# Optimization experiments

Measured on AMD Instinct MI355X. Metric: run time of the kernel, lower is better.

The kernel has to match this reference:

```python
import jax, jax.numpy as jnp
import numpy as np

B, C = 1048576, 40
ALPHA = 0.5          # additive offset so distance factor is never 0
NORMALISE = 1.0      # opt['hier_normalise']


def setup_inputs() -> dict:
    key = jax.random.key(0)
    k1, k2, k3 = jax.random.split(key, 3)
    logits = jax.random.normal(k1, (B, C), dtype=jnp.float32)
    labels = jax.random.randint(k2, (B,), 0, C, dtype=jnp.int32)
    dis_matrix = jax.random.uniform(k3, (C, C), dtype=jnp.float32)
    return {"logits": logits, "labels": labels, "dis_matrix": dis_matrix}


def reference(logits, labels, dis_matrix):
    # per-sample cross entropy (reduction='none')
    logp = jax.nn.log_softmax(logits, axis=-1)                      # [B, C]
    ce = -jnp.take_along_axis(logp, labels[:, None].astype(jnp.int32), axis=-1)[:, 0]  # [B]
    # argmax predictions (done on host in the original; pure gather here)
    pred = jnp.argmax(logits, axis=-1)                              # [B]
    # distance_factor = DIS_MATRIX[gold, pred] + alpha   (non-LCA path)
    distance_factor = dis_matrix[labels, pred] + ALPHA              # [B]
    total_loss = jnp.mean(ce * distance_factor) / NORMALISE
    return total_loss, distance_factor
```

## Files before the change

kernel.cpp:

```cpp
#include <hip/hip_runtime.h>
#include <hip/hip_bf16.h>


#define HDL_B 1048576
#define HDL_C 40
#define HDL_ALPHA 0.5f
#define HDL_BLOCK 256
#define HDL_GRID (HDL_B / HDL_BLOCK)

__global__ __launch_bounds__(HDL_BLOCK)
void hdl_main(const float* __restrict__ logits,
              const int* __restrict__ labels,
              const float* __restrict__ dis,
              float* __restrict__ out,
              double* __restrict__ wsum_global) {
    __shared__ float dls[HDL_C * HDL_C];
    __shared__ float wpart[HDL_BLOCK / 64];

    for (int i = threadIdx.x; i < HDL_C * HDL_C; i += HDL_BLOCK)
        dls[i] = dis[i];
    __syncthreads();

    const int row = blockIdx.x * HDL_BLOCK + threadIdx.x;

    const float4* rp = reinterpret_cast<const float4*>(logits + (size_t)row * HDL_C);
    float x[HDL_C];
#pragma unroll
    for (int k = 0; k < HDL_C / 4; ++k) {
        float4 t = rp[k];
        x[4 * k + 0] = t.x;
        x[4 * k + 1] = t.y;
        x[4 * k + 2] = t.z;
        x[4 * k + 3] = t.w;
    }

    float m = x[0];
    int pred = 0;
#pragma unroll
    for (int j = 1; j < HDL_C; ++j) {
        bool g = x[j] > m;
        m = g ? x[j] : m;
        pred = g ? j : pred;
    }

    const float L2E = 1.4426950408889634f;
    const float mL = m * L2E;
    float s = 0.0f;
#pragma unroll
    for (int j = 0; j < HDL_C; ++j)
        s += __builtin_amdgcn_exp2f(__builtin_fmaf(x[j], L2E, -mL));

    const int lab = labels[row];
    const float xl = logits[(size_t)row * HDL_C + lab];

    const float ce = (m - xl) + 0.69314718055994531f * __builtin_amdgcn_logf(s);

    const float df = dls[lab * HDL_C + pred] + HDL_ALPHA;
    out[1 + row] = df;

    float val = ce * df;

#pragma unroll
    for (int o = 32; o > 0; o >>= 1)
        val += __shfl_down(val, o, 64);
    const int lane = threadIdx.x & 63;
    const int wid = threadIdx.x >> 6;
    if (lane == 0) wpart[wid] = val;
    __syncthreads();
    if (threadIdx.x == 0) {
        float bs = wpart[0] + wpart[1] + wpart[2] + wpart[3];
        atomicAdd(wsum_global, (double)bs);
    }
}

__global__ void hdl_finalize(const double* __restrict__ wsum_global,
                             float* __restrict__ out) {
    out[0] = (float)(wsum_global[0] * (1.0 / (double)HDL_B));
}

extern "C" void kernel_launch(void* const* d_in, const int* in_sizes, int n_in,
                              void* d_out, int out_size, void* d_ws, size_t ws_size,
                              hipStream_t stream) {
    const float* logits = (const float*)d_in[0];
    const int*   labels = (const int*)d_in[1];
    const float* dis    = (const float*)d_in[2];
    float* out = (float*)d_out;
    double* wsum = (double*)d_ws;

    hipMemsetAsync(wsum, 0, sizeof(double), stream);

    hdl_main<<<HDL_GRID, HDL_BLOCK, 0, stream>>>(logits, labels, dis, out, wsum);
    hdl_finalize<<<1, 1, 0, stream>>>(wsum, out);
}
```

Baseline: 249.7 us.

## Stage logits through padded shared-memory tiles and replace atomic with two-pass reduction

Logits are now loaded by the whole block as consecutive float4s, so the global reads are fully coalesced, and staged through a padded shared tile in two halves before each thread pulls its own row. The label logit comes from the tile instead of a second scattered global read. The shared copy of the distance matrix is removed and it is read directly from global memory. The per-block double atomic and the memset are replaced by per-block partial sums that a 256-thread finalize kernel reduces. This adds two extra block barriers and more shared-memory traffic per block.

```diff
diff --git a/kernel.cpp b/kernel.cpp
--- a/kernel.cpp
+++ b/kernel.cpp
@@ -6,39 +6,63 @@
 #define HDL_C 40
 #define HDL_ALPHA 0.5f
 #define HDL_BLOCK 256
-#define HDL_GRID (HDL_B / HDL_BLOCK)
+#define HDL_ROWS 256
+#define HDL_GRID (HDL_B / HDL_ROWS)
+#define HDL_HALF 128
+#define HDL_PAD 41
 
 __global__ __launch_bounds__(HDL_BLOCK)
 void hdl_main(const float* __restrict__ logits,
               const int* __restrict__ labels,
               const float* __restrict__ dis,
               float* __restrict__ out,
-              double* __restrict__ wsum_global) {
-    __shared__ float dls[HDL_C * HDL_C];
+              float* __restrict__ bsum) {
+    __shared__ float tile[HDL_HALF * HDL_PAD];
     __shared__ float wpart[HDL_BLOCK / 64];
 
-    for (int i = threadIdx.x; i < HDL_C * HDL_C; i += HDL_BLOCK)
-        dls[i] = dis[i];
-    __syncthreads();
+    const int tid = threadIdx.x;
+    const int row = blockIdx.x * HDL_ROWS + tid;
 
-    const int row = blockIdx.x * HDL_BLOCK + threadIdx.x;
+    const int lab = labels[row];
 
-    const float4* rp = reinterpret_cast<const float4*>(logits + (size_t)row * HDL_C);
+    const float4* gsrc = reinterpret_cast<const float4*>(logits)
+                         + (size_t)blockIdx.x * (HDL_ROWS * HDL_C / 4);
+
     float x[HDL_C];
+    float xl = 0.0f;
+    const int myhalf = tid >> 7;
+    const int lr_mine = tid & (HDL_HALF - 1);
+
 #pragma unroll
-    for (int k = 0; k < HDL_C / 4; ++k) {
-        float4 t = rp[k];
-        x[4 * k + 0] = t.x;
-        x[4 * k + 1] = t.y;
-        x[4 * k + 2] = t.z;
-        x[4 * k + 3] = t.w;
+    for (int p = 0; p < 2; ++p) {
+#pragma unroll
+        for (int k = 0; k < 5; ++k) {
+            const int q = tid + HDL_BLOCK * k;
+            float4 v = gsrc[p * (HDL_HALF * HDL_C / 4) + q];
+            const int lr = q / 10;
+            const int c4 = q - lr * 10;
+            const int off = lr * HDL_PAD + c4 * 4;
+            tile[off + 0] = v.x;
+            tile[off + 1] = v.y;
+            tile[off + 2] = v.z;
+            tile[off + 3] = v.w;
+        }
+        __syncthreads();
+        if (myhalf == p) {
+            const int base = lr_mine * HDL_PAD;
+#pragma unroll
+            for (int j = 0; j < HDL_C; ++j)
+                x[j] = tile[base + j];
+            xl = tile[base + lab];
+        }
+        __syncthreads();
     }
 
     float m = x[0];
     int pred = 0;
 #pragma unroll
     for (int j = 1; j < HDL_C; ++j) {
-        bool g = x[j] > m;
+        const bool g = x[j] > m;
         m = g ? x[j] : m;
         pred = g ? j : pred;
     }
@@ -50,12 +74,9 @@
     for (int j = 0; j < HDL_C; ++j)
         s += __builtin_amdgcn_exp2f(__builtin_fmaf(x[j], L2E, -mL));
 
-    const int lab = labels[row];
-    const float xl = logits[(size_t)row * HDL_C + lab];
-
     const float ce = (m - xl) + 0.69314718055994531f * __builtin_amdgcn_logf(s);
 
-    const float df = dls[lab * HDL_C + pred] + HDL_ALPHA;
+    const float df = dis[lab * HDL_C + pred] + HDL_ALPHA;
     out[1 + row] = df;
 
     float val = ce * df;
@@ -63,19 +84,32 @@
 #pragma unroll
     for (int o = 32; o > 0; o >>= 1)
         val += __shfl_down(val, o, 64);
-    const int lane = threadIdx.x & 63;
-    const int wid = threadIdx.x >> 6;
+    const int lane = tid & 63;
+    const int wid = tid >> 6;
     if (lane == 0) wpart[wid] = val;
     __syncthreads();
-    if (threadIdx.x == 0) {
-        float bs = wpart[0] + wpart[1] + wpart[2] + wpart[3];
-        atomicAdd(wsum_global, (double)bs);
-    }
+    if (tid == 0)
+        bsum[blockIdx.x] = wpart[0] + wpart[1] + wpart[2] + wpart[3];
 }
 
-__global__ void hdl_finalize(const double* __restrict__ wsum_global,
-                             float* __restrict__ out) {
-    out[0] = (float)(wsum_global[0] * (1.0 / (double)HDL_B));
+__global__ __launch_bounds__(256)
+void hdl_finalize(const float* __restrict__ bsum,
+                  float* __restrict__ out) {
+    __shared__ double dpart[4];
+    const int tid = threadIdx.x;
+    double v = 0.0;
+#pragma unroll
+    for (int k = 0; k < HDL_GRID / 256; ++k)
+        v += (double)bsum[tid + 256 * k];
+#pragma unroll
+    for (int o = 32; o > 0; o >>= 1)
+        v += __shfl_down(v, o, 64);
+    if ((tid & 63) == 0) dpart[tid >> 6] = v;
+    __syncthreads();
+    if (tid == 0) {
+        const double tot = dpart[0] + dpart[1] + dpart[2] + dpart[3];
+        out[0] = (float)(tot * (1.0 / (double)HDL_B));
+    }
 }
 
 extern "C" void kernel_launch(void* const* d_in, const int* in_sizes, int n_in,
@@ -84,11 +118,9 @@
     const float* logits = (const float*)d_in[0];
     const int*   labels = (const int*)d_in[1];
     const float* dis    = (const float*)d_in[2];
-    float* out = (float*)d_out;
-    double* wsum = (double*)d_ws;
+    float* out  = (float*)d_out;
+    float* bsum = (float*)d_ws;
 
-    hipMemsetAsync(wsum, 0, sizeof(double), stream);
-
-    hdl_main<<<HDL_GRID, HDL_BLOCK, 0, stream>>>(logits, labels, dis, out, wsum);
-    hdl_finalize<<<1, 1, 0, stream>>>(wsum, out);
+    hdl_main<<<HDL_GRID, HDL_BLOCK, 0, stream>>>(logits, labels, dis, out, bsum);
+    hdl_finalize<<<1, 256, 0, stream>>>(bsum, out);
 }
```

After: 237.7 us. -4.8%, faster.
